# Optimization experiments

Measured on AMD Instinct MI355X. Metric: run time of the kernel, lower is better.

Reference implementation:

```python
import jax, jax.numpy as jnp
import numpy as np

EPS = 1e-6

def setup_inputs() -> dict:
    key = jax.random.key(0)
    k1, k2, k3 = jax.random.split(key, 3)
    B, C = 32768, 2048
    inputs = jax.random.normal(k1, (B, C), dtype=jnp.float32)
    target = jax.random.randint(k2, (B,), 0, 2047)  # targets index class columns, excluding last ('domain') column
    class_weight = jax.random.uniform(k3, (C,), dtype=jnp.float32)
    return {"input": inputs, "target": target, "class_weight": class_weight}

def reference(input, target, class_weight):
    B = input.shape[0]
    prob = jax.nn.softmax(input, axis=1)            # [B, C]
    pt = jnp.take_along_axis(prob, target[:, None], axis=1)[:, 0]  # [B] prob of target class
    pd = prob[:, -1]                                 # [B] domain prob (last column)
    w = class_weight[target]                         # [B]
    # branch pt==0: add eps inside first log; branch pt==1: scale pt by (1-eps) inside second log
    log_pt = jnp.log(jnp.where(pt == 0, pt + EPS, pt))
    log_1mpt = jnp.log(1.0 - jnp.where(pt == 1, (1.0 - EPS) * pt, pt))
    per_sample = w * (-log_pt * (1.0 - pd) - log_1mpt * pd)
    return jnp.sum(per_sample) / B
```

## Files before the change

### kernel.cpp

```cpp
#include <hip/hip_runtime.h>
#include <math.h>

#define EPS_F 1e-6f

__global__ __launch_bounds__(256) void focal_row_kernel(
    const float* __restrict__ x, const int* __restrict__ tgt,
    const float* __restrict__ cw, float* __restrict__ partial,
    int B, int C)
{
    const int wave = threadIdx.x >> 6;
    const int lane = threadIdx.x & 63;
    const int row  = blockIdx.x * 4 + wave;

    float val = 0.0f;
    if (row < B) {
        const float4* xr = (const float4*)(x + (size_t)row * (size_t)C);
        float v[32];
        float m = -3.4e38f;
#pragma unroll
        for (int i = 0; i < 8; ++i) {
            float4 f = xr[lane + 64 * i];
            v[4 * i + 0] = f.x; v[4 * i + 1] = f.y;
            v[4 * i + 2] = f.z; v[4 * i + 3] = f.w;
            m = fmaxf(m, fmaxf(fmaxf(f.x, f.y), fmaxf(f.z, f.w)));
        }
#pragma unroll
        for (int off = 32; off > 0; off >>= 1)
            m = fmaxf(m, __shfl_xor(m, off, 64));

        float s = 0.0f;
#pragma unroll
        for (int i = 0; i < 32; ++i) s += __expf(v[i] - m);
#pragma unroll
        for (int off = 32; off > 0; off >>= 1)
            s += __shfl_xor(s, off, 64);

        if (lane == 0) {
            const int t = tgt[row];
            const float xt = x[(size_t)row * (size_t)C + (size_t)t];
            const float xd = x[(size_t)row * (size_t)C + (size_t)(C-1)];
            const float inv_s = 1.0f / s;
            const float pt = __expf(xt - m) * inv_s;
            const float pd = __expf(xd - m) * inv_s;
            const float w  = cw[t];
            const float log_pt   = __logf(pt == 0.0f ? pt + EPS_F : pt);
            const float pt2      = (pt == 1.0f) ? (1.0f - EPS_F) * pt : pt;
            const float log_1mpt = __logf(1.0f - pt2);
            val = w * (-log_pt * (1.0f - pd) - log_1mpt * pd);
        }
    }

    __shared__ float sm[4];
    if (lane == 0) sm[wave] = val;
    __syncthreads();
    if (threadIdx.x == 0)
        partial[blockIdx.x] = sm[0] + sm[1] + sm[2] + sm[3];
}

__global__ __launch_bounds__(256) void reduce_partials_kernel(
    const float* __restrict__ p, float* __restrict__ out, int n, float invB)
{
    float s = 0.0f;
    for (int i = threadIdx.x; i < n; i += 256) s += p[i];
#pragma unroll
    for (int off = 32; off > 0; off >>= 1)
        s += __shfl_xor(s, off, 64);
    __shared__ float sm[4];
    const int wave = threadIdx.x >> 6;
    const int lane = threadIdx.x & 63;
    if (lane == 0) sm[wave] = s;
    __syncthreads();
    if (threadIdx.x == 0)
        out[0] = (sm[0] + sm[1] + sm[2] + sm[3]) * invB;
}

extern "C" void kernel_launch(void* const* d_in, const int* in_sizes, int n_in,
                              void* d_out, int out_size, void* d_ws, size_t ws_size,
                              hipStream_t stream)
{
    const float* x   = (const float*)d_in[0];
    const int*   tgt = (const int*)d_in[1];
    const float* cw  = (const float*)d_in[2];

    const int B = in_sizes[1];
    const int C = in_sizes[2];
    float* out = (float*)d_out;
    float* partial = (float*)d_ws;

    const int nblocks = (B + 3) / 4;
    focal_row_kernel<<<nblocks, 256, 0, stream>>>(x, tgt, cw, partial, B, C);
    reduce_partials_kernel<<<1, 256, 0, stream>>>(partial, out, nblocks,
                                                  1.0f / (float)B);
}
```

Before: 364.3 us.

## Process several rows per wave with register double-buffered prefetch of next row

Each wave now handles four rows strided across the grid and loads the next row's data into registers while computing the current row's softmax statistics. The grid shrinks by four. Partial exp sums are split into four accumulators, and the target and domain loads are issued by every lane. The aim is to hide global memory latency in this bandwidth-bound row reduction, at the cost of roughly doubling register usage and reducing the number of blocks in flight.

```diff
diff --git a/kernel.cpp b/kernel.cpp
--- a/kernel.cpp
+++ b/kernel.cpp
@@ -2,6 +2,7 @@
 #include <math.h>
 
 #define EPS_F 1e-6f
+#define RPW 4
 
 __global__ __launch_bounds__(256) void focal_row_kernel(
     const float* __restrict__ x, const int* __restrict__ tgt,
@@ -10,48 +11,78 @@
 {
     const int wave = threadIdx.x >> 6;
     const int lane = threadIdx.x & 63;
-    const int row  = blockIdx.x * 4 + wave;
+    const int wid  = blockIdx.x * 4 + wave;
+    const int nw   = gridDim.x * 4;
 
-    float val = 0.0f;
+    float acc = 0.0f;
+
+    int row = wid;
+    float4 f[8];
+    int t = 0;
     if (row < B) {
         const float4* xr = (const float4*)(x + (size_t)row * (size_t)C);
-        float v[32];
-        float m = -3.4e38f;
 #pragma unroll
-        for (int i = 0; i < 8; ++i) {
-            float4 f = xr[lane + 64 * i];
-            v[4 * i + 0] = f.x; v[4 * i + 1] = f.y;
-            v[4 * i + 2] = f.z; v[4 * i + 3] = f.w;
-            m = fmaxf(m, fmaxf(fmaxf(f.x, f.y), fmaxf(f.z, f.w)));
+        for (int i = 0; i < 8; ++i) f[i] = xr[lane + 64 * i];
+        t = tgt[row];
+    }
+
+#pragma unroll
+    for (int j = 0; j < RPW; ++j) {
+        const int nrow = row + nw;
+        float4 g[8];
+        int tn = 0;
+        if (j + 1 < RPW && nrow < B) {
+            const float4* xn = (const float4*)(x + (size_t)nrow * (size_t)C);
+#pragma unroll
+            for (int i = 0; i < 8; ++i) g[i] = xn[lane + 64 * i];
+            tn = tgt[nrow];
         }
+
+        if (row < B) {
+            const float xt = x[(size_t)row * (size_t)C + (size_t)t];
+            const float xd = x[(size_t)row * (size_t)C + (size_t)(C - 1)];
+            const float w  = cw[t];
+
+            float m = -3.4e38f;
 #pragma unroll
-        for (int off = 32; off > 0; off >>= 1)
-            m = fmaxf(m, __shfl_xor(m, off, 64));
+            for (int i = 0; i < 8; ++i)
+                m = fmaxf(m, fmaxf(fmaxf(f[i].x, f[i].y), fmaxf(f[i].z, f[i].w)));
+#pragma unroll
+            for (int off = 32; off > 0; off >>= 1)
+                m = fmaxf(m, __shfl_xor(m, off, 64));
 
-        float s = 0.0f;
+            float s0 = 0.0f, s1 = 0.0f, s2 = 0.0f, s3 = 0.0f;
 #pragma unroll
-        for (int i = 0; i < 32; ++i) s += __expf(v[i] - m);
+            for (int i = 0; i < 8; ++i) {
+                s0 += __expf(f[i].x - m);
+                s1 += __expf(f[i].y - m);
+                s2 += __expf(f[i].z - m);
+                s3 += __expf(f[i].w - m);
+            }
+            float s = (s0 + s1) + (s2 + s3);
 #pragma unroll
-        for (int off = 32; off > 0; off >>= 1)
-            s += __shfl_xor(s, off, 64);
+            for (int off = 32; off > 0; off >>= 1)
+                s += __shfl_xor(s, off, 64);
 
-        if (lane == 0) {
-            const int t = tgt[row];
-            const float xt = x[(size_t)row * (size_t)C + (size_t)t];
-            const float xd = x[(size_t)row * (size_t)C + (size_t)(C-1)];
             const float inv_s = 1.0f / s;
             const float pt = __expf(xt - m) * inv_s;
             const float pd = __expf(xd - m) * inv_s;
-            const float w  = cw[t];
             const float log_pt   = __logf(pt == 0.0f ? pt + EPS_F : pt);
             const float pt2      = (pt == 1.0f) ? (1.0f - EPS_F) * pt : pt;
             const float log_1mpt = __logf(1.0f - pt2);
-            val = w * (-log_pt * (1.0f - pd) - log_1mpt * pd);
+            acc += w * (-log_pt * (1.0f - pd) - log_1mpt * pd);
         }
+
+        if (j + 1 < RPW) {
+#pragma unroll
+            for (int i = 0; i < 8; ++i) f[i] = g[i];
+            t = tn;
+        }
+        row = nrow;
     }
 
     __shared__ float sm[4];
-    if (lane == 0) sm[wave] = val;
+    if (lane == 0) sm[wave] = acc;
     __syncthreads();
     if (threadIdx.x == 0)
         partial[blockIdx.x] = sm[0] + sm[1] + sm[2] + sm[3];
@@ -87,7 +118,7 @@
     float* out = (float*)d_out;
     float* partial = (float*)d_ws;
 
-    const int nblocks = (B + 3) / 4;
+    const int nblocks = (B + 4 * RPW - 1) / (4 * RPW);
     focal_row_kernel<<<nblocks, 256, 0, stream>>>(x, tgt, cw, partial, B, C);
     reduce_partials_kernel<<<1, 256, 0, stream>>>(partial, out, nblocks,
                                                   1.0f / (float)B);
```

Result: no change. 361.8 us (-0.7%).
